# Optimization experiments

Measured on AMD Instinct MI355X. Metric: run time of the kernel, lower is better.

The kernel has to match this reference:

```python
import jax, jax.numpy as jnp
import numpy as np

SHAPES = [(100, 100), (50, 50), (25, 25), (13, 13)]
EMBED, HEADS, LEVELS, POINTS = 256, 8, 4, 4
DH = EMBED // HEADS


def setup_inputs() -> dict:
    key = jax.random.key(0)
    ks = jax.random.split(key, 12)
    bs, nq = 4, 10000
    nv = sum(h * w for h, w in SHAPES)
    s = 0.02
    return {
        'query': jax.random.normal(ks[0], (bs, nq, EMBED), jnp.float32),
        'value': jax.random.normal(ks[1], (bs, nv, EMBED), jnp.float32),
        'reference_points': jax.random.uniform(ks[2], (bs, nq, LEVELS, 2), jnp.float32),
        'spatial_shapes': jnp.array(SHAPES, jnp.int32),
        'Wv': s * jax.random.normal(ks[3], (EMBED, EMBED), jnp.float32),
        'bv': jnp.zeros((EMBED,), jnp.float32),
        'Woff': s * jax.random.normal(ks[4], (EMBED, HEADS * LEVELS * POINTS * 2), jnp.float32),
        'boff': s * jax.random.normal(ks[5], (HEADS * LEVELS * POINTS * 2,), jnp.float32),
        'Ww': s * jax.random.normal(ks[6], (EMBED, HEADS * LEVELS * POINTS), jnp.float32),
        'bw': jnp.zeros((HEADS * LEVELS * POINTS,), jnp.float32),
        'Wo': s * jax.random.normal(ks[7], (EMBED, EMBED), jnp.float32),
        'bo': jnp.zeros((EMBED,), jnp.float32),
    }


def _msda(v, loc, aw, bs, nq):
    # v: (bs, nv, heads, dh); loc: (bs, nq, heads, L, P, 2) normalized in [0,1]
    # aw: (bs, nq, heads, L, P). Bilinear grid_sample, align_corners=False, zero padding.
    out = jnp.zeros((bs, HEADS, nq, DH), v.dtype)
    start = 0
    for l, (H, W) in enumerate(SHAPES):
        vl = v[:, start:start + H * W].transpose(0, 2, 1, 3)  # (bs, heads, H*W, dh)
        start += H * W
        locl = loc[:, :, :, l]                                # (bs, nq, heads, P, 2)
        x = locl[..., 0] * W - 0.5                            # align_corners=False mapping
        y = locl[..., 1] * H - 0.5
        x0 = jnp.floor(x); y0 = jnp.floor(y)
        fx = x - x0; fy = y - y0
        x0i = x0.astype(jnp.int32); y0i = y0.astype(jnp.int32)
        sampled = jnp.zeros((bs, HEADS, nq * POINTS, DH), v.dtype)
        for dy, wy in ((0, 1.0 - fy), (1, fy)):
            for dx, wx in ((0, 1.0 - fx), (1, fx)):
                xi = x0i + dx; yi = y0i + dy
                valid = (xi >= 0) & (xi < W) & (yi >= 0) & (yi < H)
                idx = jnp.clip(yi, 0, W and H - 1) * W + jnp.clip(xi, 0, W - 1)
                idx = jnp.clip(yi, 0, H - 1) * W + jnp.clip(xi, 0, W - 1)
                idx_t = idx.transpose(0, 2, 1, 3).reshape(bs, HEADS, nq * POINTS)
                g = jnp.take_along_axis(vl, idx_t[..., None], axis=2)  # (bs,heads,nq*P,dh)
                w = jnp.where(valid, wx * wy, 0.0).transpose(0, 2, 1, 3).reshape(bs, HEADS, -1)
                sampled = sampled + g * w[..., None]
        awl = aw[:, :, :, l].transpose(0, 2, 1, 3).reshape(bs, HEADS, nq * POINTS)
        out = out + (sampled * awl[..., None]).reshape(bs, HEADS, nq, POINTS, DH).sum(3)
    return out.transpose(0, 2, 1, 3).reshape(bs, nq, EMBED)


def reference(query, value, reference_points, spatial_shapes, Wv, bv, Woff, boff, Ww, bw, Wo, bo):
    bs, nq, _ = query.shape
    v = (value @ Wv + bv).reshape(bs, -1, HEADS, DH)
    off = (query @ Woff + boff).reshape(bs, nq, HEADS, LEVELS, POINTS, 2)
    aw = jax.nn.softmax((query @ Ww + bw).reshape(bs, nq, HEADS, LEVELS * POINTS), axis=-1)
    aw = aw.reshape(bs, nq, HEADS, LEVELS, POINTS)
    normalizer = jnp.stack([spatial_shapes[:, 1], spatial_shapes[:, 0]], -1).astype(query.dtype)  # (L,2) = (W,H)
    loc = reference_points[:, :, None, :, None, :] + off / normalizer[None, None, None, :, None, :]
    out = _msda(v, loc, aw, bs, nq)
    out = out @ Wo + bo
    return out + query  # identity residual (dropout in eval mode)
```

## Files before the change

### kernel.cpp

```cpp
#include <hip/hip_runtime.h>
#include <hip/hip_fp16.h>

#define BS     4
#define NQ     10000
#define NV     13294
#define EMBED  256
#define HEADS  8
#define LEVELS 4
#define POINTS 4
#define DH     32

#define MV_PAD 53248
#define MQ_PAD 40064

typedef __attribute__((ext_vector_type(8))) _Float16 half8;
typedef __attribute__((ext_vector_type(4))) float floatx4;

static __device__ __forceinline__ unsigned short f2h(float f) {
    __half h = __float2half(f);
    return *(unsigned short*)&h;
}
static __device__ __forceinline__ float h2f(unsigned short u) {
    __half h = *(__half*)&u;
    return __half2float(h);
}
static __device__ __forceinline__ unsigned int pk_f16(float x, float y) {
    __half2 h = __floats2half2_rn(x, y);
    unsigned int u; __builtin_memcpy(&u, &h, 4); return u;
}

static __device__ __forceinline__ void gload_lds16(const unsigned short* g, unsigned short* l) {
    __builtin_amdgcn_global_load_lds(
        (const __attribute__((address_space(1))) void*)g,
        (__attribute__((address_space(3))) void*)l,
        16, 0, 0);
}

#define CONV_BLOCKS 2048

__global__ __launch_bounds__(256) void prep_convert(
    const float* __restrict__ Wv,  const float* __restrict__ Woff,
    const float* __restrict__ boff,const float* __restrict__ Ww,
    const float* __restrict__ bw,  const float* __restrict__ Wo,
    const float* __restrict__ value, const float* __restrict__ query,
    unsigned short* __restrict__ Wvt, unsigned short* __restrict__ Wcatt,
    unsigned short* __restrict__ Wot, float* __restrict__ bcat,
    unsigned short* __restrict__ v16, unsigned short* __restrict__ q16)
{
    const int n = blockIdx.x;
    const int k = threadIdx.x;
    if (n < 896) {
        if (n < 256) {
            Wvt[n * 256 + k] = f2h(Wv[k * 256 + n]);
        } else if (n < 512) {
            Wcatt[(n - 256) * 256 + k] = f2h(Woff[k * 256 + (n - 256)]);
        } else if (n < 640) {
            Wcatt[(n - 256) * 256 + k] = f2h(Ww[k * 128 + (n - 512)]);
        } else {
            Wot[(n - 640) * 256 + k] = f2h(Wo[k * 256 + (n - 640)]);
        }
        if (n == 0) {
            for (int j = k; j < 384; j += 256)
                bcat[j] = (j < 256) ? boff[j] : bw[j - 256];
        }
        return;
    }
    const long long NV8 = (long long)BS * NV * 256 / 8;
    const long long NQ8 = (long long)BS * NQ * 256 / 8;
    const long long stride = (long long)CONV_BLOCKS * 256;
    for (long long u = (long long)(n - 896) * 256 + k; u < NV8 + NQ8; u += stride) {
        const float4* s;
        unsigned short* d;
        if (u < NV8) { s = (const float4*)value + u * 2;         d = v16 + u * 8; }
        else         { s = (const float4*)query + (u - NV8) * 2; d = q16 + (u - NV8) * 8; }
        const float4 f0 = s[0], f1 = s[1];
        uint4 o;
        o.x = pk_f16(f0.x, f0.y);
        o.y = pk_f16(f0.z, f0.w);
        o.z = pk_f16(f1.x, f1.y);
        o.w = pk_f16(f1.z, f1.w);
        *(uint4*)d = o;
    }
}

template<int MODE>
static __device__ __forceinline__ void gemm_body(
    unsigned short* As, unsigned short* Bs,
    const unsigned short* __restrict__ A, int M,
    const unsigned short* __restrict__ Bt,
    const float* __restrict__ bias,
    void* __restrict__ Cv, int ldc,
    const float* __restrict__ residual,
    int mb, int nb)
{
    const int t    = threadIdx.x;
    const int w    = t >> 6;
    const int lane = t & 63;
    const int m0 = mb * 128;
    const int n0 = nb * 128;
    const int wm = (w & 1) * 64;
    const int wn = (w >> 1) * 64;
    const int lr = lane & 15;
    const int lk = (lane >> 4) * 8;

    const int srow = w * 8 + (lane >> 3);
    const int scol = ((lane & 7) ^ (lane >> 3)) * 8;
    const unsigned short* ga = A  + (size_t)(m0 + srow) * 256 + scol;
    const unsigned short* gb = Bt + (size_t)(n0 + srow) * 256 + scol;
    unsigned short* lA = As + w * 512;
    unsigned short* lB = Bs + w * 512;

    floatx4 acc[4][4] = {};

    for (int k0 = 0; k0 < 256; k0 += 64) {
        __syncthreads();
        #pragma unroll
        for (int j = 0; j < 4; ++j) {
            gload_lds16(ga + (size_t)j * 32 * 256 + k0, lA + j * 2048);
            gload_lds16(gb + (size_t)j * 32 * 256 + k0, lB + j * 2048);
        }
        __syncthreads();

        #pragma unroll
        for (int kk = 0; kk < 64; kk += 32) {
            half8 bf[4];
            #pragma unroll
            for (int nt = 0; nt < 4; ++nt) {
                const int row = wn + nt * 16 + lr;
                const int cb  = ((kk + lk) * 2) ^ ((row & 7) << 4);
                bf[nt] = *(const half8*)((const char*)Bs + row * 128 + cb);
            }
            #pragma unroll
            for (int mt = 0; mt < 4; ++mt) {
                const int row = wm + mt * 16 + lr;
                const int cb  = ((kk + lk) * 2) ^ ((row & 7) << 4);
                const half8 af = *(const half8*)((const char*)As + row * 128 + cb);
                #pragma unroll
                for (int nt = 0; nt < 4; ++nt)
                    acc[mt][nt] = __builtin_amdgcn_mfma_f32_16x16x32_f16(af, bf[nt], acc[mt][nt], 0, 0, 0);
            }
        }
    }

    const int rbase = m0 + wm + (lane >> 4) * 4;
    #pragma unroll
    for (int nt = 0; nt < 4; ++nt) {
        const int col = n0 + wn + nt * 16 + lr;
        const float bb_ = bias[col];
        #pragma unroll
        for (int mt = 0; mt < 4; ++mt) {
            #pragma unroll
            for (int r = 0; r < 4; ++r) {
                const int row = rbase + mt * 16 + r;
                if (row < M) {
                    float val = acc[mt][nt][r] + bb_;
                    if (MODE == 2) val += residual[(size_t)row * ldc + col];
                    if (MODE == 0)
                        ((unsigned short*)Cv)[(size_t)row * ldc + col] = f2h(val);
                    else
                        ((float*)Cv)[(size_t)row * ldc + col] = val;
                }
            }
        }
    }
}

__global__ __launch_bounds__(256) void gemm_fused12(
    const unsigned short* __restrict__ v16, const unsigned short* __restrict__ q16,
    const unsigned short* __restrict__ Wvt, const unsigned short* __restrict__ Wcatt,
    const float* __restrict__ bv, const float* __restrict__ bcat,
    unsigned short* __restrict__ vout, unsigned short* __restrict__ projout)
{
    __shared__ __align__(16) unsigned short As[128 * 64];
    __shared__ __align__(16) unsigned short Bs[128 * 64];
    const unsigned int xcd = blockIdx.x & 7u, kk = blockIdx.x >> 3;
    const unsigned int wg = (xcd < 3u ? xcd * 222u : 3u * 222u + (xcd - 3u) * 221u) + kk;
    if (wg < 832u) {
        gemm_body<0>(As, Bs, v16, BS * NV, Wvt, bv, vout, 256, nullptr,
                     (int)(wg >> 1), (int)(wg & 1));
    } else {
        const unsigned int b2 = wg - 832u;
        gemm_body<0>(As, Bs, q16, BS * NQ, Wcatt, bcat, projout, 384, nullptr,
                     (int)(b2 / 3u), (int)(b2 % 3u));
    }
}

__global__ __launch_bounds__(256) void gemm_out(
    const unsigned short* __restrict__ msda, const unsigned short* __restrict__ Wot,
    const float* __restrict__ bo, float* __restrict__ out,
    const float* __restrict__ query)
{
    __shared__ __align__(16) unsigned short As[128 * 64];
    __shared__ __align__(16) unsigned short Bs[128 * 64];
    const unsigned int xcd = blockIdx.x & 7u, kk = blockIdx.x >> 3;
    const unsigned int wg = (xcd < 2u ? xcd * 79u : 2u * 79u + (xcd - 2u) * 78u) + kk;
    gemm_body<2>(As, Bs, msda, BS * NQ, Wot, bo, out, 256, query,
                 (int)(wg >> 1), (int)(wg & 1));
}

__global__ __launch_bounds__(256) void msda_sample(
    const unsigned short* __restrict__ v,
    const unsigned short* __restrict__ proj,
    const float* __restrict__ rp,
    unsigned short* __restrict__ out)
{
    __shared__ __align__(16) unsigned int taps[4 * 1056];

    const int wave = threadIdx.x >> 6;
    const int lane = threadIdx.x & 63;
    const int q = blockIdx.x * 4 + wave;
    const int b = blockIdx.y;
    const int rowq = b * NQ + q;
    const unsigned short* prow = proj + (size_t)rowq * 384;

    const int hA = lane >> 3;
    const int li = lane & 7;
    const int c0 = li * 2;

    const ushort2 lgu = *(const ushort2*)&prow[256 + hA * 16 + c0];
    const float lgx = h2f(lgu.x), lgy = h2f(lgu.y);
    float mx = fmaxf(lgx, lgy);
    mx = fmaxf(mx, __shfl_xor(mx, 1));
    mx = fmaxf(mx, __shfl_xor(mx, 2));
    mx = fmaxf(mx, __shfl_xor(mx, 4));
    const float e0 = __expf(lgx - mx);
    const float e1 = __expf(lgy - mx);
    float ssum = e0 + e1;
    ssum += __shfl_xor(ssum, 1);
    ssum += __shfl_xor(ssum, 2);
    ssum += __shfl_xor(ssum, 4);
    const float inv = 1.0f / ssum;

    const int l = c0 >> 2;
    const int Wl = (l == 0) ? 100 : (l == 1) ? 50 : (l == 2) ? 25 : 13;
    const int st = (l == 0) ? 0 : (l == 1) ? 10000 : (l == 2) ? 12500 : 13125;
    const int Hl = Wl;
    const float fW = (float)Wl, fH = (float)Hl;

    const float2 rxy = *(const float2*)&rp[((size_t)rowq * 4 + l) * 2];

    unsigned int* tbase = taps + wave * 1056 + hA * 132;

    #pragma unroll
    for (int cc = 0; cc < 2; ++cc) {
        const int c = c0 + cc;
        const ushort2 oxyu = *(const ushort2*)&prow[hA * 32 + c * 2];
        const float ox = h2f(oxyu.x), oy = h2f(oxyu.y);
        const float aww = (cc ? e1 : e0) * inv;
        const float x = fmaf(rxy.x, fW, ox) - 0.5f;
        const float y = fmaf(rxy.y, fH, oy) - 0.5f;
        const float x0f = floorf(x), y0f = floorf(y);
        const float fx = x - x0f, fy = y - y0f;
        const int ix = (int)x0f, iy = (int)y0f;
        const float wxv[2] = {1.f - fx, fx};
        const float wyv[2] = {1.f - fy, fy};

        unsigned int offv[4]; float wv_[4];
        #pragma unroll
        for (int tp = 0; tp < 4; ++tp) {
            const int dy = tp >> 1, dx = tp & 1;
            const int xi = ix + dx, yi = iy + dy;
            const bool ok = (xi >= 0) && (xi < Wl) && (yi >= 0) && (yi < Hl);
            const int cx = min(max(xi, 0), Wl - 1);
            const int cy = min(max(yi, 0), Hl - 1);
            offv[tp] = (unsigned int)(st + cy * Wl + cx) * 512u + (unsigned int)hA * 64u;
            wv_[tp]  = ok ? wyv[dy] * wxv[dx] * aww : 0.f;
        }
        const uint4 e0v = make_uint4(offv[0], offv[1], pk_f16(wv_[0], wv_[0]), pk_f16(wv_[1], wv_[1]));
        const uint4 e1v = make_uint4(offv[2], offv[3], pk_f16(wv_[2], wv_[2]), pk_f16(wv_[3], wv_[3]));
        *(uint4*)&tbase[c * 8]     = e0v;
        *(uint4*)&tbase[c * 8 + 4] = e1v;
    }

    asm volatile("s_waitcnt lgkmcnt(0)" ::: "memory");

    const int h = lane >> 3;
    const unsigned int lane_off = (unsigned int)(lane & 7) * 8u;
    const char* vbase = (const char*)v + (size_t)b * NV * 512;
    const uint4* tp4 = (const uint4*)(taps + wave * 1056 + h * 132);

    __half2 a01 = __floats2half2_rn(0.f, 0.f);
    __half2 a23 = __floats2half2_rn(0.f, 0.f);
    #pragma unroll 8
    for (int j = 0; j < 32; ++j) {
        const uint4 ee = tp4[j];
        const uint2 g0 = *(const uint2*)(vbase + (ee.x + lane_off));
        const uint2 g1 = *(const uint2*)(vbase + (ee.y + lane_off));
        __half2 w0, w1, v0, v1, v2, v3;
        __builtin_memcpy(&w0, &ee.z, 4);
        __builtin_memcpy(&w1, &ee.w, 4);
        __builtin_memcpy(&v0, &g0.x, 4);
        __builtin_memcpy(&v1, &g0.y, 4);
        __builtin_memcpy(&v2, &g1.x, 4);
        __builtin_memcpy(&v3, &g1.y, 4);
        a01 = __hfma2(v0, w0, a01);
        a23 = __hfma2(v1, w0, a23);
        a01 = __hfma2(v2, w1, a01);
        a23 = __hfma2(v3, w1, a23);
    }

    uint2 o;
    __builtin_memcpy(&o.x, &a01, 4);
    __builtin_memcpy(&o.y, &a23, 4);
    *(uint2*)&out[(size_t)rowq * 256 + h * 32 + (lane & 7) * 4] = o;
}

extern "C" void kernel_launch(void* const* d_in, const int* in_sizes, int n_in,
                              void* d_out, int out_size, void* d_ws, size_t ws_size,
                              hipStream_t stream) {
    const float* query = (const float*)d_in[0];
    const float* value = (const float*)d_in[1];
    const float* rp    = (const float*)d_in[2];
    const float* Wv    = (const float*)d_in[4];
    const float* bv    = (const float*)d_in[5];
    const float* Woff  = (const float*)d_in[6];
    const float* boff  = (const float*)d_in[7];
    const float* Ww    = (const float*)d_in[8];
    const float* bw    = (const float*)d_in[9];
    const float* Wo    = (const float*)d_in[10];
    const float* bo    = (const float*)d_in[11];
    float* out = (float*)d_out;

    const int Mq = BS * NQ;

    char* ws = (char*)d_ws;
    const size_t SZ_MSDA = (size_t)MQ_PAD * 256 * 2;
    const size_t SZ_VIN  = (size_t)MV_PAD * 256 * 2;
    const size_t SZ_QIN  = (size_t)MQ_PAD * 256 * 2;
    const size_t SZ_VPR  = (size_t)BS * NV * 256 * 2;
    const size_t SZ_PROJ = (size_t)Mq * 384 * 2;

    unsigned short* msda  = (unsigned short*)(ws);
    unsigned short* v16   = (unsigned short*)(ws + SZ_MSDA);
    unsigned short* q16   = (unsigned short*)(ws + SZ_MSDA + SZ_VIN);
    unsigned short* v_prj = (unsigned short*)(ws + SZ_MSDA + SZ_VIN + SZ_QIN);
    unsigned short* proj  = (unsigned short*)(ws + SZ_MSDA + SZ_VIN + SZ_QIN + SZ_VPR);
    char* wp = ws + SZ_MSDA + SZ_VIN + SZ_QIN + SZ_VPR + SZ_PROJ;
    unsigned short* Wvt   = (unsigned short*)(wp);
    unsigned short* Wcatt = (unsigned short*)(wp + 256 * 256 * 2);
    unsigned short* Wot   = (unsigned short*)(wp + 256 * 256 * 2 + 384 * 256 * 2);
    float*          bcat  = (float*)(wp + 256 * 256 * 2 + 384 * 256 * 2 + 256 * 256 * 2);

    prep_convert<<<896 + CONV_BLOCKS, 256, 0, stream>>>(
        Wv, Woff, boff, Ww, bw, Wo, value, query,
        Wvt, Wcatt, Wot, bcat, v16, q16);

    gemm_fused12<<<832 + 939, 256, 0, stream>>>(
        v16, q16, Wvt, Wcatt, bv, bcat, v_prj, proj);

    msda_sample<<<dim3(NQ / 4, BS), 256, 0, stream>>>(v_prj, proj, rp, msda);

    gemm_out<<<626, 256, 0, stream>>>(msda, Wot, bo, out, query);
}
```

Baseline: 316.0 us.

## Store projected values head-major and schedule sampling blocks per head

The value-projection GEMM now writes its fp16 output in a (batch, head, position, dh) layout instead of row-major (position, embed). The sampling kernel is remapped so that each block handles one head and batch for 32 queries, with block ids interleaved so consecutive blocks cover different heads. The goal is to keep each block's gathers inside a compact per-head value slab (64 bytes per position), which improves L2 and cache locality on the MI355X's split XCDs. In exchange, the GEMM epilogue does scattered 2-byte stores with integer divides, and the softmax and offset loads become strided across queries.

After: 317.5 us. No clear change (+0.5%).

```diff
diff --git a/kernel.cpp b/kernel.cpp
--- a/kernel.cpp
+++ b/kernel.cpp
@@ -155,10 +155,16 @@
                 if (row < M) {
                     float val = acc[mt][nt][r] + bb_;
                     if (MODE == 2) val += residual[(size_t)row * ldc + col];
-                    if (MODE == 0)
+                    if (MODE == 0) {
                         ((unsigned short*)Cv)[(size_t)row * ldc + col] = f2h(val);
-                    else
+                    } else if (MODE == 3) {
+                        const int b_ = row / NV;
+                        const int s_ = row - b_ * NV;
+                        const int h_ = col >> 5, d_ = col & 31;
+                        ((unsigned short*)Cv)[(((size_t)b_ * 8 + h_) * NV + s_) * 32 + d_] = f2h(val);
+                    } else {
                         ((float*)Cv)[(size_t)row * ldc + col] = val;
+                    }
                 }
             }
         }
@@ -176,7 +182,7 @@
     const unsigned int xcd = blockIdx.x & 7u, kk = blockIdx.x >> 3;
     const unsigned int wg = (xcd < 3u ? xcd * 222u : 3u * 222u + (xcd - 3u) * 221u) + kk;
     if (wg < 832u) {
-        gemm_body<0>(As, Bs, v16, BS * NV, Wvt, bv, vout, 256, nullptr,
+        gemm_body<3>(As, Bs, v16, BS * NV, Wvt, bv, vout, 256, nullptr,
                      (int)(wg >> 1), (int)(wg & 1));
     } else {
         const unsigned int b2 = wg - 832u;
@@ -206,18 +212,22 @@
 {
     __shared__ __align__(16) unsigned int taps[4 * 1056];
 
+    const unsigned int bid = blockIdx.x;
+    const int h      = (int)(bid & 7u);
+    const int b      = (int)((bid >> 3) & 3u);
+    const int qchunk = (int)(bid >> 5);
     const int wave = threadIdx.x >> 6;
     const int lane = threadIdx.x & 63;
-    const int q = blockIdx.x * 4 + wave;
-    const int b = blockIdx.y;
-    const int rowq = b * NQ + q;
+    const int qi   = lane >> 3;
+    const int li   = lane & 7;
+    const int q    = qchunk * 32 + wave * 8 + qi;
+    const bool qok = q < NQ;
+    const int rowq = b * NQ + (qok ? q : 0);
     const unsigned short* prow = proj + (size_t)rowq * 384;
 
-    const int hA = lane >> 3;
-    const int li = lane & 7;
     const int c0 = li * 2;
 
-    const ushort2 lgu = *(const ushort2*)&prow[256 + hA * 16 + c0];
+    const ushort2 lgu = *(const ushort2*)&prow[256 + h * 16 + c0];
     const float lgx = h2f(lgu.x), lgy = h2f(lgu.y);
     float mx = fmaxf(lgx, lgy);
     mx = fmaxf(mx, __shfl_xor(mx, 1));
@@ -239,12 +249,12 @@
 
     const float2 rxy = *(const float2*)&rp[((size_t)rowq * 4 + l) * 2];
 
-    unsigned int* tbase = taps + wave * 1056 + hA * 132;
+    unsigned int* tbase = taps + wave * 1056 + qi * 132;
 
     #pragma unroll
     for (int cc = 0; cc < 2; ++cc) {
         const int c = c0 + cc;
-        const ushort2 oxyu = *(const ushort2*)&prow[hA * 32 + c * 2];
+        const ushort2 oxyu = *(const ushort2*)&prow[h * 32 + c * 2];
         const float ox = h2f(oxyu.x), oy = h2f(oxyu.y);
         const float aww = (cc ? e1 : e0) * inv;
         const float x = fmaf(rxy.x, fW, ox) - 0.5f;
@@ -263,7 +273,7 @@
             const bool ok = (xi >= 0) && (xi < Wl) && (yi >= 0) && (yi < Hl);
             const int cx = min(max(xi, 0), Wl - 1);
             const int cy = min(max(yi, 0), Hl - 1);
-            offv[tp] = (unsigned int)(st + cy * Wl + cx) * 512u + (unsigned int)hA * 64u;
+            offv[tp] = (unsigned int)(st + cy * Wl + cx) * 64u;
             wv_[tp]  = ok ? wyv[dy] * wxv[dx] * aww : 0.f;
         }
         const uint4 e0v = make_uint4(offv[0], offv[1], pk_f16(wv_[0], wv_[0]), pk_f16(wv_[1], wv_[1]));
@@ -274,10 +284,9 @@
 
     asm volatile("s_waitcnt lgkmcnt(0)" ::: "memory");
 
-    const int h = lane >> 3;
-    const unsigned int lane_off = (unsigned int)(lane & 7) * 8u;
-    const char* vbase = (const char*)v + (size_t)b * NV * 512;
-    const uint4* tp4 = (const uint4*)(taps + wave * 1056 + h * 132);
+    const unsigned int lane_off = (unsigned int)li * 8u;
+    const char* vbase = (const char*)v + ((size_t)b * 8 + h) * (size_t)NV * 64;
+    const uint4* tp4 = (const uint4*)(taps + wave * 1056 + qi * 132);
 
     __half2 a01 = __floats2half2_rn(0.f, 0.f);
     __half2 a23 = __floats2half2_rn(0.f, 0.f);
@@ -299,10 +308,12 @@
         a23 = __hfma2(v3, w1, a23);
     }
 
-    uint2 o;
-    __builtin_memcpy(&o.x, &a01, 4);
-    __builtin_memcpy(&o.y, &a23, 4);
-    *(uint2*)&out[(size_t)rowq * 256 + h * 32 + (lane & 7) * 4] = o;
+    if (qok) {
+        uint2 o;
+        __builtin_memcpy(&o.x, &a01, 4);
+        __builtin_memcpy(&o.y, &a23, 4);
+        *(uint2*)&out[(size_t)rowq * 256 + h * 32 + li * 4] = o;
+    }
 }
 
 extern "C" void kernel_launch(void* const* d_in, const int* in_sizes, int n_in,
@@ -348,7 +359,7 @@
     gemm_fused12<<<832 + 939, 256, 0, stream>>>(
         v16, q16, Wvt, Wcatt, bv, bcat, v_prj, proj);
 
-    msda_sample<<<dim3(NQ / 4, BS), 256, 0, stream>>>(v_prj, proj, rp, msda);
+    msda_sample<<<313 * 32, 256, 0, stream>>>(v_prj, proj, rp, msda);
 
     gemm_out<<<626, 256, 0, stream>>>(msda, Wot, bo, out, query);
 }
```
